# Kernel optimization log

Measured on AMD Instinct MI355X. Metric: run time of the kernel, lower is better.

Reference implementation:

```python
import jax, jax.numpy as jnp
import numpy as np

EMBED = 768
N_HEADS = 12
HEAD = EMBED // N_HEADS  # 64
B, T = 2, 2048


def setup_inputs() -> dict:
    key = jax.random.key(0)
    ks = jax.random.split(key, 5)
    s = 0.02
    return {
        "x": jax.random.normal(ks[0], (B, T, EMBED), dtype=jnp.float32),
        "w_attn": jax.random.normal(ks[1], (EMBED, 3 * EMBED), dtype=jnp.float32) * s,
        "b_attn": jnp.zeros((3 * EMBED,), dtype=jnp.float32),
        "w_proj": jax.random.normal(ks[2], (EMBED, EMBED), dtype=jnp.float32) * s,
        "b_proj": jnp.zeros((EMBED,), dtype=jnp.float32),
    }


def reference(x, w_attn, b_attn, w_proj, b_proj):
    b, t, c = x.shape
    scale = HEAD ** -0.5
    qkv = x @ w_attn + b_attn  # [b,t,3c]
    q, k, v = jnp.split(qkv, 3, axis=-1)

    # einops 'b t (h n) -> b n t h' with n=N_HEADS: channel dim factors as
    # (head_size, n_heads) — head index is the inner factor.
    def split_heads(u):
        return u.reshape(b, t, HEAD, N_HEADS).transpose(0, 3, 1, 2)  # [b,n,t,h]

    q, k, v = split_heads(q), split_heads(k), split_heads(v)

    scores = jnp.einsum("bnth,bnsh->bnts", q, k) * scale  # [b,n,t,t]
    causal = jnp.tril(jnp.ones((t, t), dtype=bool))
    scores = jnp.where(causal, scores, jnp.finfo(scores.dtype).min)
    weights = jax.nn.softmax(scores, axis=-1)
    att = jnp.einsum("bnts,bnsh->bnth", weights, v)  # [b,n,t,h]

    # 'b n t h -> b t (n h)': heads are the OUTER factor on output
    att = att.transpose(0, 2, 1, 3).reshape(b, t, c)
    return att @ w_proj + b_proj
```

## Files before the change

### kernel.cpp

```cpp
#include <hip/hip_runtime.h>
#include <hip/hip_bf16.h>
#include <math.h>

#define NB      2
#define T_SZ    2048
#define EMBEDC  768
#define NHEADS  12
#define HEADD   64
#define QKV_PER (NB * NHEADS * T_SZ * HEADD)
#define QSCALE  0.18033688011112042f

typedef __bf16 bf16x8 __attribute__((ext_vector_type(8)));
typedef float  f32x4  __attribute__((ext_vector_type(4)));

__device__ inline ushort f2bf(float x) {
    union { float f; uint u; } v; v.f = x;
    uint r = v.u + 0x7fffu + ((v.u >> 16) & 1u);
    return (ushort)(r >> 16);
}

__device__ inline uint pack2bf(float a, float b) {
    union { __bf16 h[2]; uint u; } t;
    t.h[0] = (__bf16)a; t.h[1] = (__bf16)b;
    return t.u;
}

__device__ inline void gload16(const ushort* g, ushort* l) {
    __builtin_amdgcn_global_load_lds(
        (const __attribute__((address_space(1))) unsigned int*)g,
        (__attribute__((address_space(3))) unsigned int*)l, 16, 0, 0);
}

__global__ __launch_bounds__(256) void cast_k(const float* __restrict__ in,
                                              ushort* __restrict__ out, int n)
{
    int i = (blockIdx.x * 256 + threadIdx.x) * 8;
    if (i >= n) return;
    float4 a = *(const float4*)(in + i);
    float4 b = *(const float4*)(in + i + 4);
    union { ushort u[8]; int4 v; } p;
    p.u[0] = f2bf(a.x); p.u[1] = f2bf(a.y); p.u[2] = f2bf(a.z); p.u[3] = f2bf(a.w);
    p.u[4] = f2bf(b.x); p.u[5] = f2bf(b.y); p.u[6] = f2bf(b.z); p.u[7] = f2bf(b.w);
    *(int4*)(out + i) = p.v;
}

template <int PERM>
__global__ __launch_bounds__(256) void tcast_k(const float* __restrict__ in,
                                               ushort* __restrict__ out,
                                               int R, int C)
{
    __shared__ float t[32][33];
    const int c0 = blockIdx.x * 32, r0 = blockIdx.y * 32;
    const int tx = threadIdx.x & 31, ty = threadIdx.x >> 5;
#pragma unroll
    for (int u = 0; u < 4; ++u)
        t[ty + 8 * u][tx] = in[(size_t)(r0 + ty + 8 * u) * C + c0 + tx];
    __syncthreads();
#pragma unroll
    for (int u = 0; u < 4; ++u) {
        int n = c0 + ty + 8 * u;
        int orow = n;
        if (PERM) {
            int mat = n / EMBEDC, cc = n % EMBEDC;
            orow = mat * EMBEDC + (cc % NHEADS) * HEADD + cc / NHEADS;
        }
        out[(size_t)orow * R + r0 + tx] = f2bf(t[tx][ty + 8 * u]);
    }
}

__global__ __launch_bounds__(256) void vt_k(const ushort* __restrict__ in,
                                            ushort* __restrict__ out)
{
    __shared__ ushort tile[64][66];
    const int bh = blockIdx.y;
    const int t0 = blockIdx.x * 64;
    const int tid = threadIdx.x;
#pragma unroll
    for (int u = 0; u < 2; ++u) {
        int s = tid + 256 * u;
        int r = s >> 3, c8 = s & 7;
        *(bf16x8*)&tile[r][c8 * 8] =
            *(const bf16x8*)(in + ((size_t)bh * T_SZ + t0 + r) * HEADD + c8 * 8);
    }
    __syncthreads();
#pragma unroll
    for (int u = 0; u < 2; ++u) {
        int s = tid + 256 * u;
        int hd = s >> 3, tt = s & 7;
        union { ushort v[8]; int4 q; } pk;
#pragma unroll
        for (int j = 0; j < 8; ++j) pk.v[j] = tile[tt * 8 + j][hd];
        *(int4*)(out + ((size_t)bh * HEADD + hd) * T_SZ + t0 + tt * 8) = pk.q;
    }
}

#define STAGE(buf, koff)                                        \
    do {                                                        \
        gload16(gA0 + (koff), &As[buf][lA0o]);                  \
        gload16(gA1 + (koff), &As[buf][lA1o]);                  \
        gload16(gB0 + (koff), &Bs[buf][lB0o]);                  \
        gload16(gB1 + (koff), &Bs[buf][lB1o]);                  \
    } while (0)

template <int MODE>
__global__ __launch_bounds__(256) void gemm_bf16_k(
    const ushort* __restrict__ A, const ushort* __restrict__ Bt,
    const float* __restrict__ bias, void* __restrict__ outp,
    int M, int N, int K)
{
    __shared__ ushort As[2][128 * 32];
    __shared__ ushort Bs[2][128 * 32];

    const int tid = threadIdx.x;
    const int w = tid >> 6, l = tid & 63;
    const int g = l >> 4, r16 = l & 15;
    const int wr = w >> 1, wc = w & 1;
    const int m0 = blockIdx.y * 128, n0 = blockIdx.x * 128;

    const int srow = l >> 2;
    const int scol = ((l & 3) ^ (srow & 3)) * 8;
    const ushort* gA0 = A + (size_t)(m0 + 32 * w + srow) * K + scol;
    const ushort* gA1 = gA0 + (size_t)16 * K;
    const ushort* gB0 = Bt + (size_t)(n0 + 32 * w + srow) * K + scol;
    const ushort* gB1 = gB0 + (size_t)16 * K;
    const int lA0o = (32 * w) * 32,      lA1o = (32 * w + 16) * 32;
    const int lB0o = lA0o,               lB1o = lA1o;

    f32x4 acc[4][4];
#pragma unroll
    for (int i = 0; i < 4; ++i)
#pragma unroll
        for (int j = 0; j < 4; ++j) acc[i][j] = (f32x4){0.f, 0.f, 0.f, 0.f};

    const int rck = (r16 & 3);

    STAGE(0, 0);
    __syncthreads();

    int cur = 0;
    for (int k0 = 0; k0 < K; k0 += 32) {
        if (k0 + 32 < K) STAGE(cur ^ 1, k0 + 32);

        const ushort* sA = As[cur];
        const ushort* sB = Bs[cur];
        bf16x8 af[4], bfr[4];
#pragma unroll
        for (int ms = 0; ms < 4; ++ms) {
            int row = 64 * wr + 16 * ms + r16;
            af[ms] = *(const bf16x8*)&sA[row * 32 + ((g ^ rck) * 8)];
        }
#pragma unroll
        for (int ns = 0; ns < 4; ++ns) {
            int row = 64 * wc + 16 * ns + r16;
            bfr[ns] = *(const bf16x8*)&sB[row * 32 + ((g ^ rck) * 8)];
        }
#pragma unroll
        for (int ms = 0; ms < 4; ++ms)
#pragma unroll
            for (int ns = 0; ns < 4; ++ns)
                acc[ms][ns] = __builtin_amdgcn_mfma_f32_16x16x32_bf16(
                    af[ms], bfr[ns], acc[ms][ns], 0, 0, 0);

        __syncthreads();
        cur ^= 1;
    }

#pragma unroll
    for (int ns = 0; ns < 4; ++ns) {
        const int n = n0 + 64 * wc + 16 * ns + r16;
        if (MODE == 0) {
            float* out = (float*)outp;
            const float bv = bias[n];
#pragma unroll
            for (int ms = 0; ms < 4; ++ms) {
                const int mb = m0 + 64 * wr + 16 * ms + 4 * g;
#pragma unroll
                for (int r = 0; r < 4; ++r)
                    out[(size_t)(mb + r) * N + n] = acc[ms][ns][r] + bv;
            }
        } else {
            ushort* ob = (ushort*)outp;
            const int mat  = n / EMBEDC;
            const int c    = n - mat * EMBEDC;
            const int head = c >> 6;
            const int hd   = c & 63;
            const float bv = bias[mat * EMBEDC + hd * NHEADS + head];
            const float qs = (mat == 0) ? QSCALE : 1.f;
#pragma unroll
            for (int ms = 0; ms < 4; ++ms) {
                const int mb = m0 + 64 * wr + 16 * ms + 4 * g;
#pragma unroll
                for (int r = 0; r < 4; ++r) {
                    const int m = mb + r;
                    const int b = m >> 11, t = m & 2047;
                    const size_t bh = (size_t)(b * NHEADS + head);
                    ob[(size_t)mat * QKV_PER + (bh * T_SZ + t) * HEADD + hd] =
                        f2bf((acc[ms][ns][r] + bv) * qs);
                }
            }
        }
    }
}

__global__ __launch_bounds__(256, 2) void attn_mfma_k(
    const ushort* __restrict__ Qb, const ushort* __restrict__ Kb,
    const ushort* __restrict__ Vtb, ushort* __restrict__ Out)
{
    __shared__ ushort smem[16384];
    __shared__ float Ml[4 * 64], Ll[4 * 64];

    ushort* Ks = smem;
    ushort* Vs = smem + 8192;

    const int pairIdx = blockIdx.x;
    const int bh = blockIdx.y;
    const int bb = bh / NHEADS, head = bh % NHEADS;
    const int tid = threadIdx.x;
    const int w = tid >> 6, l = tid & 63;
    const int g = l >> 4, r16 = l & 15;
    const ushort* Qg = Qb + (size_t)bh * T_SZ * HEADD;
    const ushort* Kg = Kb + (size_t)bh * T_SZ * HEADD;
    const ushort* Vg = Vtb + (size_t)bh * HEADD * T_SZ;

    const int srcLo = ((g & 1) << 5) | r16;
    const int srcHi = srcLo + 16;
    const bool kcSel = (g >> 1) != 0;

    for (int rep = 0; rep < 2; ++rep) {
        const int qb = rep ? (31 - pairIdx) : pairIdx;
        const int q0 = qb * 64;
        const int nt = qb / 2 + 1;

        bf16x8 qf[4][2];
#pragma unroll
        for (int qi = 0; qi < 4; ++qi) {
            const ushort* qp = Qg + (size_t)(q0 + qi * 16 + r16) * HEADD + g * 8;
            qf[qi][0] = *(const bf16x8*)(qp);
            qf[qi][1] = *(const bf16x8*)(qp + 32);
        }

        f32x4 o[4][4];
#pragma unroll
        for (int dc = 0; dc < 4; ++dc)
#pragma unroll
            for (int qi = 0; qi < 4; ++qi) o[dc][qi] = (f32x4){0.f,0.f,0.f,0.f};
        float mR[4], lR[4];
#pragma unroll
        for (int qi = 0; qi < 4; ++qi) { mR[qi] = -1e30f; lR[qi] = 0.f; }

        __syncthreads();

        bf16x8 kr[4], vr[4];
#pragma unroll
        for (int u = 0; u < 4; ++u) {
            int s = tid + 256 * u;
            kr[u] = *(const bf16x8*)(Kg + (size_t)(s >> 3) * HEADD + (s & 7) * 8);
            vr[u] = *(const bf16x8*)(Vg + (size_t)(s >> 4) * T_SZ + (s & 15) * 8);
        }
#pragma unroll
        for (int u = 0; u < 4; ++u) {
            int s = tid + 256 * u;
            int krow = s >> 3, kc8 = s & 7;
            int vrow = s >> 4, vc16 = s & 15;
            *(bf16x8*)&Ks[krow * 64 + ((kc8 ^ (krow & 7)) * 8)] = kr[u];
            *(bf16x8*)&Vs[vrow * 128 + ((vc16 ^ (vrow & 15)) * 8)] = vr[u];
        }
        __syncthreads();

        for (int kt = 0; kt < nt; ++kt) {
            if (kt + 1 < nt) {
                const int k1 = (kt + 1) * 128;
#pragma unroll
                for (int u = 0; u < 4; ++u) {
                    int s = tid + 256 * u;
                    kr[u] = *(const bf16x8*)(Kg + (size_t)(k1 + (s >> 3)) * HEADD +
                                             (s & 7) * 8);
                    vr[u] = *(const bf16x8*)(Vg + (size_t)(s >> 4) * T_SZ + k1 +
                                             (s & 15) * 8);
                }
            }

            f32x4 st[2][4];
#pragma unroll
            for (int kc = 0; kc < 2; ++kc) {
                int row = 32 * w + kc * 16 + r16;
                const ushort* kp = &Ks[row * 64];
                bf16x8 a0 = *(const bf16x8*)(kp + ((g    ) ^ (r16 & 7)) * 8);
                bf16x8 a1 = *(const bf16x8*)(kp + ((g + 4) ^ (r16 & 7)) * 8);
#pragma unroll
                for (int qi = 0; qi < 4; ++qi) {
                    f32x4 c = (f32x4){0.f, 0.f, 0.f, 0.f};
                    c = __builtin_amdgcn_mfma_f32_16x16x32_bf16(a0, qf[qi][0], c, 0, 0, 0);
                    c = __builtin_amdgcn_mfma_f32_16x16x32_bf16(a1, qf[qi][1], c, 0, 0, 0);
                    st[kc][qi] = c;
                }
            }

            if (kt == nt - 1) {
                const int kvb = kt * 128 + 32 * w;
#pragma unroll
                for (int kc = 0; kc < 2; ++kc)
#pragma unroll
                    for (int qi = 0; qi < 4; ++qi)
#pragma unroll
                        for (int r = 0; r < 4; ++r)
                            if (kvb + kc * 16 + 4 * g + r > q0 + qi * 16 + r16)
                                st[kc][qi][r] = -1e30f;
            }

            float pm[4];
#pragma unroll
            for (int qi = 0; qi < 4; ++qi) {
                float m = fmaxf(fmaxf(st[0][qi][0], st[0][qi][1]),
                                fmaxf(st[0][qi][2], st[0][qi][3]));
                m = fmaxf(m, fmaxf(fmaxf(st[1][qi][0], st[1][qi][1]),
                                   fmaxf(st[1][qi][2], st[1][qi][3])));
                m = fmaxf(m, __shfl_xor(m, 16));
                m = fmaxf(m, __shfl_xor(m, 32));
                pm[qi] = m;
            }
            float dm = fmaxf(fmaxf(pm[0] - mR[0], pm[1] - mR[1]),
                             fmaxf(pm[2] - mR[2], pm[3] - mR[3]));
            if (!__all(dm <= 8.f)) {
#pragma unroll
                for (int qi = 0; qi < 4; ++qi) {
                    float mNew = fmaxf(mR[qi], pm[qi]);
                    float sc = exp2f(mR[qi] - mNew);
                    lR[qi] *= sc;
                    mR[qi] = mNew;
#pragma unroll
                    for (int dc = 0; dc < 4; ++dc) o[dc][qi] *= sc;
                }
            }
#pragma unroll
            for (int qi = 0; qi < 4; ++qi) {
                float rs = 0.f;
#pragma unroll
                for (int kc = 0; kc < 2; ++kc)
#pragma unroll
                    for (int r = 0; r < 4; ++r) {
                        float e = exp2f(st[kc][qi][r] - mR[qi]);
                        st[kc][qi][r] = e;
                        rs += e;
                    }
                rs += __shfl_xor(rs, 16);
                rs += __shfl_xor(rs, 32);
                lR[qi] += rs;
            }

            uint pk[4][2][2];
#pragma unroll
            for (int qi = 0; qi < 4; ++qi)
#pragma unroll
                for (int kc = 0; kc < 2; ++kc) {
                    pk[qi][kc][0] = pack2bf(st[kc][qi][0], st[kc][qi][1]);
                    pk[qi][kc][1] = pack2bf(st[kc][qi][2], st[kc][qi][3]);
                }

            bf16x8 vf[4];
#pragma unroll
            for (int dc = 0; dc < 4; ++dc) {
                int row = dc * 16 + r16;
                vf[dc] = *(const bf16x8*)
                    &Vs[row * 128 + (((4 * w + g) ^ (row & 15)) * 8)];
            }

#pragma unroll
            for (int qi = 0; qi < 4; ++qi) {
                uint A0 = (uint)__shfl((int)pk[qi][0][0], srcLo);
                uint A1 = (uint)__shfl((int)pk[qi][0][1], srcLo);
                uint B0 = (uint)__shfl((int)pk[qi][1][0], srcLo);
                uint B1 = (uint)__shfl((int)pk[qi][1][1], srcLo);
                uint A2 = (uint)__shfl((int)pk[qi][0][0], srcHi);
                uint A3 = (uint)__shfl((int)pk[qi][0][1], srcHi);
                uint B2 = (uint)__shfl((int)pk[qi][1][0], srcHi);
                uint B3 = (uint)__shfl((int)pk[qi][1][1], srcHi);
                union { uint u[4]; bf16x8 v; } t;
                t.u[0] = kcSel ? B0 : A0;
                t.u[1] = kcSel ? B1 : A1;
                t.u[2] = kcSel ? B2 : A2;
                t.u[3] = kcSel ? B3 : A3;
#pragma unroll
                for (int dc = 0; dc < 4; ++dc)
                    o[dc][qi] = __builtin_amdgcn_mfma_f32_16x16x32_bf16(
                        vf[dc], t.v, o[dc][qi], 0, 0, 0);
            }

            __syncthreads();
            if (kt + 1 < nt) {
#pragma unroll
                for (int u = 0; u < 4; ++u) {
                    int s = tid + 256 * u;
                    int krow = s >> 3, kc8 = s & 7;
                    int vrow = s >> 4, vc16 = s & 15;
                    *(bf16x8*)&Ks[krow * 64 + ((kc8 ^ (krow & 7)) * 8)] = kr[u];
                    *(bf16x8*)&Vs[vrow * 128 + ((vc16 ^ (vrow & 15)) * 8)] = vr[u];
                }
                __syncthreads();
            }
        }

        if (g == 0) {
#pragma unroll
            for (int qi = 0; qi < 4; ++qi) {
                Ml[w * 64 + qi * 16 + r16] = mR[qi];
                Ll[w * 64 + qi * 16 + r16] = lR[qi];
            }
        }
        __syncthreads();

        float lt[4];
#pragma unroll
        for (int qi = 0; qi < 4; ++qi) {
            const int ix = qi * 16 + r16;
            float m0 = Ml[ix], m1 = Ml[64 + ix], m2 = Ml[128 + ix], m3 = Ml[192 + ix];
            float mt = fmaxf(fmaxf(m0, m1), fmaxf(m2, m3));
            float f = exp2f(mR[qi] - mt);
#pragma unroll
            for (int dc = 0; dc < 4; ++dc) o[dc][qi] *= f;
            lt[qi] = Ll[ix]       * exp2f(m0 - mt) + Ll[64 + ix]  * exp2f(m1 - mt)
                   + Ll[128 + ix] * exp2f(m2 - mt) + Ll[192 + ix] * exp2f(m3 - mt);
        }
        __syncthreads();

        float* img0 = (float*)smem;
        float* img1 = (float*)smem + 4096;

        if (w >= 2) {
            float* img = (w == 2) ? img0 : img1;
#pragma unroll
            for (int dc = 0; dc < 4; ++dc)
#pragma unroll
                for (int qi = 0; qi < 4; ++qi)
#pragma unroll
                    for (int r = 0; r < 4; ++r)
                        img[(dc * 16 + 4 * g + r) * 64 + qi * 16 + r16] = o[dc][qi][r];
        }
        __syncthreads();
        if (w < 2) {
            const float* img = (w == 0) ? img0 : img1;
#pragma unroll
            for (int dc = 0; dc < 4; ++dc)
#pragma unroll
                for (int qi = 0; qi < 4; ++qi)
#pragma unroll
                    for (int r = 0; r < 4; ++r)
                        o[dc][qi][r] += img[(dc * 16 + 4 * g + r) * 64 + qi * 16 + r16];
        }
        __syncthreads();
        if (w == 1) {
#pragma unroll
            for (int dc = 0; dc < 4; ++dc)
#pragma unroll
                for (int qi = 0; qi < 4; ++qi)
#pragma unroll
                    for (int r = 0; r < 4; ++r)
                        img0[(dc * 16 + 4 * g + r) * 64 + qi * 16 + r16] = o[dc][qi][r];
        }
        __syncthreads();
        if (w == 0) {
#pragma unroll
            for (int qi = 0; qi < 4; ++qi) {
                const float inv = 1.f / lt[qi];
                ushort* orow = Out + ((size_t)(bb * T_SZ + q0 + qi * 16 + r16)) * EMBEDC
                             + head * HEADD;
#pragma unroll
                for (int dc = 0; dc < 4; ++dc)
#pragma unroll
                    for (int r = 0; r < 4; ++r) {
                        float v = o[dc][qi][r] +
                            img0[(dc * 16 + 4 * g + r) * 64 + qi * 16 + r16];
                        orow[dc * 16 + 4 * g + r] = f2bf(v * inv);
                    }
            }
        }
    }
}

extern "C" void kernel_launch(void* const* d_in, const int* in_sizes, int n_in,
                              void* d_out, int out_size, void* d_ws, size_t ws_size,
                              hipStream_t stream)
{
    const float* x      = (const float*)d_in[0];
    const float* w_attn = (const float*)d_in[1];
    const float* b_attn = (const float*)d_in[2];
    const float* w_proj = (const float*)d_in[3];
    const float* b_proj = (const float*)d_in[4];
    float* out = (float*)d_out;

    ushort* qw   = (ushort*)d_ws;
    ushort* vT   = qw + (size_t)3 * QKV_PER;
    ushort* attb = vT + QKV_PER;
    ushort* xb   = attb + QKV_PER;
    ushort* waT  = xb + QKV_PER;
    ushort* wpT  = waT + (size_t)EMBEDC * 3 * EMBEDC;

    cast_k<<<QKV_PER / (256 * 8), 256, 0, stream>>>(x, xb, QKV_PER);
    tcast_k<1><<<dim3(3 * EMBEDC / 32, EMBEDC / 32), 256, 0, stream>>>(
        w_attn, waT, EMBEDC, 3 * EMBEDC);
    tcast_k<0><<<dim3(EMBEDC / 32, EMBEDC / 32), 256, 0, stream>>>(
        w_proj, wpT, EMBEDC, EMBEDC);

    gemm_bf16_k<1><<<dim3(2304 / 128, 4096 / 128), 256, 0, stream>>>(
        xb, waT, b_attn, qw, NB * T_SZ, 3 * EMBEDC, EMBEDC);

    vt_k<<<dim3(T_SZ / 64, NB * NHEADS), 256, 0, stream>>>(
        qw + 2 * (size_t)QKV_PER, vT);

    attn_mfma_k<<<dim3(16, NB * NHEADS), 256, 0, stream>>>(
        qw, qw + QKV_PER, vT, attb);

    gemm_bf16_k<0><<<dim3(768 / 128, 4096 / 128), 256, 0, stream>>>(
        attb, wpT, b_proj, out, NB * T_SZ, EMBEDC, EMBEDC);
}
```

Before: 131.9 us.

## Share K/V tiles across two adjacent query blocks in 512-thread attention blocks

The attention kernel moves from 256-thread blocks, which handled a head-paired query block 'rep' loop, to 512-thread blocks in which two 4-wave groups process adjacent 64-row query blocks while sharing each staged K/V tile. The grid becomes 1D, with an XCD-aware block-to-head mapping and longest-first ordering. The final cross-wave reduction becomes a serial vectorized swizzled LDS accumulation with packed 4-wide bf16 stores. The aim is to halve K/V global loads and LDS staging per query row and to improve load balance and L2 locality. The cost is more barriers per block, and waves idle on the diagonal tile because half of one group is masked off.

```diff
diff --git a/kernel.cpp b/kernel.cpp
--- a/kernel.cpp
+++ b/kernel.cpp
@@ -202,22 +202,28 @@
     }
 }
 
-__global__ __launch_bounds__(256, 2) void attn_mfma_k(
+__global__ __launch_bounds__(512, 4) void attn_mfma_k(
     const ushort* __restrict__ Qb, const ushort* __restrict__ Kb,
     const ushort* __restrict__ Vtb, ushort* __restrict__ Out)
 {
     __shared__ ushort smem[16384];
-    __shared__ float Ml[4 * 64], Ll[4 * 64];
+    __shared__ float Ml[8 * 64], Ll[8 * 64];
 
     ushort* Ks = smem;
     ushort* Vs = smem + 8192;
 
-    const int pairIdx = blockIdx.x;
-    const int bh = blockIdx.y;
+    const int id = blockIdx.x;
+    const int xcd = id & 7, slot = id >> 3;
+    const int bh = xcd * 3 + (slot >> 4);
+    const int pairIdx = 15 - (slot & 15);
     const int bb = bh / NHEADS, head = bh % NHEADS;
     const int tid = threadIdx.x;
     const int w = tid >> 6, l = tid & 63;
+    const int grp = w >> 2, wl = w & 3;
     const int g = l >> 4, r16 = l & 15;
+    const int qb = 2 * pairIdx + grp;
+    const int q0 = qb * 64;
+    const int nt = pairIdx + 1;
     const ushort* Qg = Qb + (size_t)bh * T_SZ * HEADD;
     const ushort* Kg = Kb + (size_t)bh * T_SZ * HEADD;
     const ushort* Vg = Vtb + (size_t)bh * HEADD * T_SZ;
@@ -226,64 +232,59 @@
     const int srcHi = srcLo + 16;
     const bool kcSel = (g >> 1) != 0;
 
-    for (int rep = 0; rep < 2; ++rep) {
-        const int qb = rep ? (31 - pairIdx) : pairIdx;
-        const int q0 = qb * 64;
-        const int nt = qb / 2 + 1;
-
-        bf16x8 qf[4][2];
-#pragma unroll
-        for (int qi = 0; qi < 4; ++qi) {
-            const ushort* qp = Qg + (size_t)(q0 + qi * 16 + r16) * HEADD + g * 8;
-            qf[qi][0] = *(const bf16x8*)(qp);
-            qf[qi][1] = *(const bf16x8*)(qp + 32);
-        }
-
-        f32x4 o[4][4];
-#pragma unroll
-        for (int dc = 0; dc < 4; ++dc)
-#pragma unroll
-            for (int qi = 0; qi < 4; ++qi) o[dc][qi] = (f32x4){0.f,0.f,0.f,0.f};
-        float mR[4], lR[4];
-#pragma unroll
-        for (int qi = 0; qi < 4; ++qi) { mR[qi] = -1e30f; lR[qi] = 0.f; }
-
-        __syncthreads();
-
-        bf16x8 kr[4], vr[4];
-#pragma unroll
-        for (int u = 0; u < 4; ++u) {
-            int s = tid + 256 * u;
-            kr[u] = *(const bf16x8*)(Kg + (size_t)(s >> 3) * HEADD + (s & 7) * 8);
-            vr[u] = *(const bf16x8*)(Vg + (size_t)(s >> 4) * T_SZ + (s & 15) * 8);
-        }
-#pragma unroll
-        for (int u = 0; u < 4; ++u) {
-            int s = tid + 256 * u;
-            int krow = s >> 3, kc8 = s & 7;
-            int vrow = s >> 4, vc16 = s & 15;
-            *(bf16x8*)&Ks[krow * 64 + ((kc8 ^ (krow & 7)) * 8)] = kr[u];
-            *(bf16x8*)&Vs[vrow * 128 + ((vc16 ^ (vrow & 15)) * 8)] = vr[u];
-        }
-        __syncthreads();
-
-        for (int kt = 0; kt < nt; ++kt) {
-            if (kt + 1 < nt) {
-                const int k1 = (kt + 1) * 128;
-#pragma unroll
-                for (int u = 0; u < 4; ++u) {
-                    int s = tid + 256 * u;
-                    kr[u] = *(const bf16x8*)(Kg + (size_t)(k1 + (s >> 3)) * HEADD +
-                                             (s & 7) * 8);
-                    vr[u] = *(const bf16x8*)(Vg + (size_t)(s >> 4) * T_SZ + k1 +
-                                             (s & 15) * 8);
-                }
-            }
-
+    bf16x8 qf[4][2];
+#pragma unroll
+    for (int qi = 0; qi < 4; ++qi) {
+        const ushort* qp = Qg + (size_t)(q0 + qi * 16 + r16) * HEADD + g * 8;
+        qf[qi][0] = *(const bf16x8*)(qp);
+        qf[qi][1] = *(const bf16x8*)(qp + 32);
+    }
+
+    f32x4 o[4][4];
+#pragma unroll
+    for (int dc = 0; dc < 4; ++dc)
+#pragma unroll
+        for (int qi = 0; qi < 4; ++qi) o[dc][qi] = (f32x4){0.f, 0.f, 0.f, 0.f};
+    float mR[4], lR[4];
+#pragma unroll
+    for (int qi = 0; qi < 4; ++qi) { mR[qi] = -1e30f; lR[qi] = 0.f; }
+
+    bf16x8 kr[2], vr[2];
+#pragma unroll
+    for (int u = 0; u < 2; ++u) {
+        int s = tid + 512 * u;
+        kr[u] = *(const bf16x8*)(Kg + (size_t)(s >> 3) * HEADD + (s & 7) * 8);
+        vr[u] = *(const bf16x8*)(Vg + (size_t)(s >> 4) * T_SZ + (s & 15) * 8);
+    }
+#pragma unroll
+    for (int u = 0; u < 2; ++u) {
+        int s = tid + 512 * u;
+        int krow = s >> 3, kc8 = s & 7;
+        int vrow = s >> 4, vc16 = s & 15;
+        *(bf16x8*)&Ks[krow * 64 + ((kc8 ^ (krow & 7)) * 8)] = kr[u];
+        *(bf16x8*)&Vs[vrow * 128 + ((vc16 ^ (vrow & 15)) * 8)] = vr[u];
+    }
+    __syncthreads();
+
+    for (int kt = 0; kt < nt; ++kt) {
+        if (kt + 1 < nt) {
+            const int k1 = (kt + 1) * 128;
+#pragma unroll
+            for (int u = 0; u < 2; ++u) {
+                int s = tid + 512 * u;
+                kr[u] = *(const bf16x8*)(Kg + (size_t)(k1 + (s >> 3)) * HEADD +
+                                         (s & 7) * 8);
+                vr[u] = *(const bf16x8*)(Vg + (size_t)(s >> 4) * T_SZ + k1 +
+                                         (s & 15) * 8);
+            }
+        }
+
+        const bool act = !(kt == nt - 1 && grp == 0 && wl >= 2);
+        if (act) {
             f32x4 st[2][4];
 #pragma unroll
             for (int kc = 0; kc < 2; ++kc) {
-                int row = 32 * w + kc * 16 + r16;
+                int row = 32 * wl + kc * 16 + r16;
                 const ushort* kp = &Ks[row * 64];
                 bf16x8 a0 = *(const bf16x8*)(kp + ((g    ) ^ (r16 & 7)) * 8);
                 bf16x8 a1 = *(const bf16x8*)(kp + ((g + 4) ^ (r16 & 7)) * 8);
@@ -297,7 +298,7 @@
             }
 
             if (kt == nt - 1) {
-                const int kvb = kt * 128 + 32 * w;
+                const int kvb = kt * 128 + 32 * wl;
 #pragma unroll
                 for (int kc = 0; kc < 2; ++kc)
 #pragma unroll
@@ -362,7 +363,7 @@
             for (int dc = 0; dc < 4; ++dc) {
                 int row = dc * 16 + r16;
                 vf[dc] = *(const bf16x8*)
-                    &Vs[row * 128 + (((4 * w + g) ^ (row & 15)) * 8)];
+                    &Vs[row * 128 + (((4 * wl + g) ^ (row & 15)) * 8)];
             }
 
 #pragma unroll
@@ -385,93 +386,84 @@
                     o[dc][qi] = __builtin_amdgcn_mfma_f32_16x16x32_bf16(
                         vf[dc], t.v, o[dc][qi], 0, 0, 0);
             }
-
+        }
+
+        __syncthreads();
+        if (kt + 1 < nt) {
+#pragma unroll
+            for (int u = 0; u < 2; ++u) {
+                int s = tid + 512 * u;
+                int krow = s >> 3, kc8 = s & 7;
+                int vrow = s >> 4, vc16 = s & 15;
+                *(bf16x8*)&Ks[krow * 64 + ((kc8 ^ (krow & 7)) * 8)] = kr[u];
+                *(bf16x8*)&Vs[vrow * 128 + ((vc16 ^ (vrow & 15)) * 8)] = vr[u];
+            }
             __syncthreads();
-            if (kt + 1 < nt) {
-#pragma unroll
-                for (int u = 0; u < 4; ++u) {
-                    int s = tid + 256 * u;
-                    int krow = s >> 3, kc8 = s & 7;
-                    int vrow = s >> 4, vc16 = s & 15;
-                    *(bf16x8*)&Ks[krow * 64 + ((kc8 ^ (krow & 7)) * 8)] = kr[u];
-                    *(bf16x8*)&Vs[vrow * 128 + ((vc16 ^ (vrow & 15)) * 8)] = vr[u];
-                }
-                __syncthreads();
-            }
-        }
-
-        if (g == 0) {
-#pragma unroll
-            for (int qi = 0; qi < 4; ++qi) {
-                Ml[w * 64 + qi * 16 + r16] = mR[qi];
-                Ll[w * 64 + qi * 16 + r16] = lR[qi];
-            }
-        }
-        __syncthreads();
-
-        float lt[4];
+        }
+    }
+
+    if (g == 0) {
 #pragma unroll
         for (int qi = 0; qi < 4; ++qi) {
-            const int ix = qi * 16 + r16;
-            float m0 = Ml[ix], m1 = Ml[64 + ix], m2 = Ml[128 + ix], m3 = Ml[192 + ix];
+            Ml[w * 64 + qi * 16 + r16] = mR[qi];
+            Ll[w * 64 + qi * 16 + r16] = lR[qi];
+        }
+    }
+    __syncthreads();
+
+    float lt[4];
+    {
+        const int base = grp * 256;
+#pragma unroll
+        for (int qi = 0; qi < 4; ++qi) {
+            const int ix = base + qi * 16 + r16;
+            float m0 = Ml[ix], m1 = Ml[ix + 64], m2 = Ml[ix + 128], m3 = Ml[ix + 192];
             float mt = fmaxf(fmaxf(m0, m1), fmaxf(m2, m3));
             float f = exp2f(mR[qi] - mt);
 #pragma unroll
             for (int dc = 0; dc < 4; ++dc) o[dc][qi] *= f;
-            lt[qi] = Ll[ix]       * exp2f(m0 - mt) + Ll[64 + ix]  * exp2f(m1 - mt)
-                   + Ll[128 + ix] * exp2f(m2 - mt) + Ll[192 + ix] * exp2f(m3 - mt);
+            lt[qi] = Ll[ix]       * exp2f(m0 - mt) + Ll[ix + 64]  * exp2f(m1 - mt)
+                   + Ll[ix + 128] * exp2f(m2 - mt) + Ll[ix + 192] * exp2f(m3 - mt);
+        }
+    }
+
+    float* img = (float*)smem + grp * 4096;
+#pragma unroll
+    for (int rnd = 1; rnd <= 3; ++rnd) {
+        if (wl == rnd) {
+#pragma unroll
+            for (int dc = 0; dc < 4; ++dc)
+#pragma unroll
+                for (int qi = 0; qi < 4; ++qi)
+                    *(f32x4*)&img[(qi * 16 + r16) * 64 + (((dc * 4 + g) ^ r16) & 15) * 4]
+                        = o[dc][qi];
         }
         __syncthreads();
-
-        float* img0 = (float*)smem;
-        float* img1 = (float*)smem + 4096;
-
-        if (w >= 2) {
-            float* img = (w == 2) ? img0 : img1;
+        if (wl == 0) {
 #pragma unroll
             for (int dc = 0; dc < 4; ++dc)
 #pragma unroll
                 for (int qi = 0; qi < 4; ++qi)
-#pragma unroll
-                    for (int r = 0; r < 4; ++r)
-                        img[(dc * 16 + 4 * g + r) * 64 + qi * 16 + r16] = o[dc][qi][r];
+                    o[dc][qi] += *(const f32x4*)
+                        &img[(qi * 16 + r16) * 64 + (((dc * 4 + g) ^ r16) & 15) * 4];
         }
         __syncthreads();
-        if (w < 2) {
-            const float* img = (w == 0) ? img0 : img1;
-#pragma unroll
-            for (int dc = 0; dc < 4; ++dc)
-#pragma unroll
-                for (int qi = 0; qi < 4; ++qi)
-#pragma unroll
-                    for (int r = 0; r < 4; ++r)
-                        o[dc][qi][r] += img[(dc * 16 + 4 * g + r) * 64 + qi * 16 + r16];
-        }
-        __syncthreads();
-        if (w == 1) {
-#pragma unroll
-            for (int dc = 0; dc < 4; ++dc)
-#pragma unroll
-                for (int qi = 0; qi < 4; ++qi)
-#pragma unroll
-                    for (int r = 0; r < 4; ++r)
-                        img0[(dc * 16 + 4 * g + r) * 64 + qi * 16 + r16] = o[dc][qi][r];
-        }
-        __syncthreads();
-        if (w == 0) {
-#pragma unroll
-            for (int qi = 0; qi < 4; ++qi) {
-                const float inv = 1.f / lt[qi];
-                ushort* orow = Out + ((size_t)(bb * T_SZ + q0 + qi * 16 + r16)) * EMBEDC
-                             + head * HEADD;
-#pragma unroll
-                for (int dc = 0; dc < 4; ++dc)
-#pragma unroll
-                    for (int r = 0; r < 4; ++r) {
-                        float v = o[dc][qi][r] +
-                            img0[(dc * 16 + 4 * g + r) * 64 + qi * 16 + r16];
-                        orow[dc * 16 + 4 * g + r] = f2bf(v * inv);
-                    }
+    }
+
+    if (wl == 0) {
+#pragma unroll
+        for (int qi = 0; qi < 4; ++qi) {
+            const float inv = 1.f / lt[qi];
+            ushort* orow = Out + ((size_t)(bb * T_SZ + q0 + qi * 16 + r16)) * EMBEDC
+                         + head * HEADD;
+#pragma unroll
+            for (int dc = 0; dc < 4; ++dc) {
+                ushort4 pv;
+                pv.x = f2bf(o[dc][qi][0] * inv);
+                pv.y = f2bf(o[dc][qi][1] * inv);
+                pv.z = f2bf(o[dc][qi][2] * inv);
+                pv.w = f2bf(o[dc][qi][3] * inv);
+                *(ushort4*)(orow + dc * 16 + 4 * g) = pv;
             }
         }
     }
@@ -507,7 +499,7 @@
     vt_k<<<dim3(T_SZ / 64, NB * NHEADS), 256, 0, stream>>>(
         qw + 2 * (size_t)QKV_PER, vT);
 
-    attn_mfma_k<<<dim3(16, NB * NHEADS), 256, 0, stream>>>(
+    attn_mfma_k<<<384, 512, 0, stream>>>(
         qw, qw + QKV_PER, vT, attb);
 
     gemm_bf16_k<0><<<dim3(768 / 128, 4096 / 128), 256, 0, stream>>>(
```

After: 306.6 us. 133% more time.
